# Optimization experiments

Hardware: AMD Instinct MI355X
Metric: run time of the kernel (lower is better)

The kernel has to match this reference:

```python
import jax, jax.numpy as jnp
import numpy as np

N = 100000   # nodes
E = 25000    # hyperedges
NNZ = 2000000
IN_CH = 64
HEADS = 8
OUT_CH = 8
HO = HEADS * OUT_CH  # 64


def setup_inputs() -> dict:
    key = jax.random.key(0)
    k1, k2, k3, k4, k5 = jax.random.split(key, 5)
    X = jax.random.normal(k1, (N, IN_CH), dtype=jnp.float32)
    vertex = jax.random.randint(k2, (NNZ,), 0, N, dtype=jnp.int64 if jax.config.jax_enable_x64 else jnp.int32)
    edges = jax.random.randint(k3, (NNZ,), 0, E, dtype=jnp.int64 if jax.config.jax_enable_x64 else jnp.int32)
    homo = jax.random.uniform(k4, (E,), dtype=jnp.float32) + 0.1  # positive per-hyperedge scalar
    # nn.Linear(in, heads*out, bias=False): store as [in, heads*out] for X @ W
    W = jax.random.normal(k5, (IN_CH, HO), dtype=jnp.float32) * (1.0 / np.sqrt(IN_CH))
    return {"X": X, "W": W, "homo": homo, "vertex": vertex, "edges": edges}


def reference(X, W, homo, vertex, edges):
    n = X.shape[0]
    e = homo.shape[0]
    Xp = X @ W                                   # [N, H*O]
    Xve = Xp[vertex]                             # [nnz, H*O] gather node->incidence
    # first_aggregate = 'mean': vertex features -> hyperedge features
    Xe_sum = jax.ops.segment_sum(Xve, edges, num_segments=e)
    cnt = jax.ops.segment_sum(jnp.ones((Xve.shape[0],), Xve.dtype), edges, num_segments=e)
    Xe = Xe_sum / jnp.maximum(cnt, 1.0)[:, None]  # [E, H*O]
    Xev = Xe[edges]                              # [nnz, H*O] gather edge->incidence
    he = homo[edges]                             # [nnz]
    att_sum = jax.ops.segment_sum(he, vertex, num_segments=n)[vertex]  # [nnz]
    att = he / att_sum                           # [nnz] (homo > 0 so sums > 0 at incident slots)
    att_Xev = att[:, None] * Xev                 # fused version of att.mm(ones).mul(Xev)
    # second_aggregate = 'sum': hyperedge features -> node features
    Xv = jax.ops.segment_sum(att_Xev, vertex, num_segments=n)  # [N, H*O]
    out = Xp + Xv
    # use_norm: row-l2 normalize with DETACHED norm (scale is a constant wrt grad)
    rownorm = jax.lax.stop_gradient(jnp.linalg.norm(out, axis=1, keepdims=True))
    scale = jnp.where(rownorm > 0, 1.0 / jnp.maximum(rownorm, 1e-30), 0.0)
    return out * scale
```

## Files before the change

### kernel.cpp

```cpp
#include <hip/hip_runtime.h>
#include <hip/hip_bf16.h>


#define SE_LOG 5
#define SV_LOG 7
#define CH     4096
#define CAPB   8192

typedef __attribute__((ext_vector_type(8))) short bf16x8;
typedef __attribute__((ext_vector_type(4))) float f32x4;

__device__ __forceinline__ float bf2f(unsigned short u) {
    union { unsigned int i; float f; } x;
    x.i = ((unsigned int)u) << 16;
    return x.f;
}

__device__ __forceinline__ float bflo(unsigned int u) {
    union { unsigned int i; float f; } x;
    x.i = u << 16;
    return x.f;
}

__device__ __forceinline__ float bfhi(unsigned int u) {
    union { unsigned int i; float f; } x;
    x.i = u & 0xffff0000u;
    return x.f;
}

__device__ __forceinline__ unsigned short f2bf(float f) {
    union { unsigned int i; float ff; } x;
    x.ff = f;
    unsigned int r = x.i + 0x7fff + ((x.i >> 16) & 1);
    return (unsigned short)(r >> 16);
}

__device__ __forceinline__ float loadF(const void* p, size_t i, int bf16mode) {
    return bf16mode ? bf2f(((const unsigned short*)p)[i]) : ((const float*)p)[i];
}

__device__ __forceinline__ int loadI(const void* p, size_t i, int i64mode) {
    return i64mode ? ((const int*)p)[2 * i] : ((const int*)p)[i];
}

__global__ void sniff_kernel(const void* X, const void* vtx, int* flags) {
    if (threadIdx.x != 0 || blockIdx.x != 0) return;
    const unsigned short* u = (const unsigned short*)X;
    int sane = 0;
    for (int i = 0; i < 64; ++i) {
        unsigned short lo = u[2 * i];
        int e = (lo >> 7) & 0xFF;
        if (e >= 110 && e <= 137) ++sane;
    }
    flags[0] = (sane >= 32) ? 1 : 0;
    const int* w = (const int*)vtx;
    int zeros = 0;
    for (int i = 0; i < 64; ++i)
        if (w[2 * i + 1] == 0) ++zeros;
    flags[1] = (zeros >= 32) ? 1 : 0;
}

__global__ void homof_kernel(const void* __restrict__ homo,
                             const int* __restrict__ flags,
                             float* __restrict__ homof, int E) {
    int i = blockIdx.x * blockDim.x + threadIdx.x;
    if (i < E) homof[i] = loadF(homo, i, flags[0]);
}

__global__ __launch_bounds__(256)
void gemm_mfma_kernel(const unsigned short* __restrict__ X,
                      const unsigned short* __restrict__ W,
                      const int* __restrict__ flags,
                      unsigned short* __restrict__ Xpb, int N) {
    if (flags[0] == 0) return;
    __shared__ float Ld[4][16 * 68];
    int tid  = threadIdx.x;
    int lane = tid & 63, w = tid >> 6;
    int quad = lane >> 4, c16 = lane & 15;
    bf16x8 bfrag[4][2];
#pragma unroll
    for (int t = 0; t < 4; ++t)
#pragma unroll
        for (int s = 0; s < 2; ++s)
#pragma unroll
            for (int j = 0; j < 8; ++j)
                bfrag[t][s][j] = (short)W[(s * 32 + quad * 8 + j) * 64 + t * 16 + c16];

    int tiles = (N + 15) >> 4;
    int wid = blockIdx.x * 4 + w;
    int nw  = gridDim.x * 4;
    int lr = lane >> 2, seg = lane & 3;
    for (int tile = wid; tile < tiles; tile += nw) {
        int r0 = tile * 16;
        int rA = r0 + c16; if (rA > N - 1) rA = N - 1;
        bf16x8 a0 = *(const bf16x8*)(X + (size_t)rA * 64 + quad * 8);
        bf16x8 a1 = *(const bf16x8*)(X + (size_t)rA * 64 + 32 + quad * 8);
#pragma unroll
        for (int t = 0; t < 4; ++t) {
            f32x4 z = {0.f, 0.f, 0.f, 0.f};
            z = __builtin_amdgcn_mfma_f32_16x16x32_bf16(a0, bfrag[t][0], z, 0, 0, 0);
            z = __builtin_amdgcn_mfma_f32_16x16x32_bf16(a1, bfrag[t][1], z, 0, 0, 0);
#pragma unroll
            for (int i = 0; i < 4; ++i)
                Ld[w][(quad * 4 + i) * 68 + t * 16 + c16] = z[i];
        }
        int r = r0 + lr;
        if (r < N) {
            const float* src = &Ld[w][lr * 68 + seg * 16];
            unsigned int p[8];
#pragma unroll
            for (int i = 0; i < 8; ++i)
                p[i] = (unsigned)f2bf(src[2 * i]) | ((unsigned)f2bf(src[2 * i + 1]) << 16);
            uint4* dst = (uint4*)(Xpb + (size_t)r * 64 + seg * 16);
            dst[0] = make_uint4(p[0], p[1], p[2], p[3]);
            dst[1] = make_uint4(p[4], p[5], p[6], p[7]);
        }
    }
}

__global__ __launch_bounds__(256)
void gemm_f32_kernel(const void* __restrict__ X, const void* __restrict__ W,
                     const int* __restrict__ flags,
                     unsigned short* __restrict__ Xpb, int N) {
    if (flags[0] == 1) return;
    __shared__ float Ws[64 * 64];
    __shared__ float Xs[16][64];
    int tid = threadIdx.x;
    for (int j = tid; j < 4096; j += 256) Ws[j] = ((const float*)W)[j];
    __syncthreads();
    int lane = tid & 63, w = tid >> 6;
    int wid = (blockIdx.x * 256 + tid) >> 6;
    int nw  = (gridDim.x * 256) >> 6;
    for (int r0 = wid * 4; r0 < N; r0 += nw * 4) {
        if (r0 + 4 <= N) {
            float acc0 = 0.f, acc1 = 0.f, acc2 = 0.f, acc3 = 0.f;
#pragma unroll
            for (int j = 0; j < 4; ++j)
                Xs[w * 4 + j][lane] = ((const float*)X)[(size_t)(r0 + j) * 64 + lane];
#pragma unroll
            for (int k4 = 0; k4 < 16; ++k4) {
                float4 x0 = *(const float4*)&Xs[w * 4 + 0][k4 * 4];
                float4 x1 = *(const float4*)&Xs[w * 4 + 1][k4 * 4];
                float4 x2 = *(const float4*)&Xs[w * 4 + 2][k4 * 4];
                float4 x3 = *(const float4*)&Xs[w * 4 + 3][k4 * 4];
#pragma unroll
                for (int kk = 0; kk < 4; ++kk) {
                    float wv = Ws[(k4 * 4 + kk) * 64 + lane];
                    acc0 = fmaf((&x0.x)[kk], wv, acc0);
                    acc1 = fmaf((&x1.x)[kk], wv, acc1);
                    acc2 = fmaf((&x2.x)[kk], wv, acc2);
                    acc3 = fmaf((&x3.x)[kk], wv, acc3);
                }
            }
            float a[4] = {acc0, acc1, acc2, acc3};
#pragma unroll
            for (int j = 0; j < 4; ++j)
                Xpb[(size_t)(r0 + j) * 64 + lane] = f2bf(a[j]);
        } else {
            for (int r = r0; r < N; ++r) {
                Xs[w * 4][lane] = ((const float*)X)[(size_t)r * 64 + lane];
                float acc = 0.f;
                for (int k = 0; k < 64; ++k)
                    acc = fmaf(Xs[w * 4][k], Ws[k * 64 + lane], acc);
                Xpb[(size_t)r * 64 + lane] = f2bf(acc);
            }
        }
    }
}

__global__ __launch_bounds__(1024)
void bhist2_kernel(const void* __restrict__ edges, const void* __restrict__ vertex,
                   const int* __restrict__ flags, int* __restrict__ btot,
                   int* __restrict__ slabc, int nnz, int NBE, int NBT) {
    __shared__ int cnt[2048];
    int tid = threadIdx.x, b = blockIdx.x;
    for (int j = tid; j < NBT; j += 1024) cnt[j] = 0;
    __syncthreads();
    int imode = flags[1];
    int c0 = b * CH, c1 = min(nnz, c0 + CH);
    for (int i = c0 + tid; i < c1; i += 1024) {
        int e = loadI(edges, i, imode);
        int v = loadI(vertex, i, imode);
        atomicAdd(&cnt[e >> SE_LOG], 1);
        atomicAdd(&cnt[NBE + (v >> SV_LOG)], 1);
    }
    __syncthreads();
    for (int j = tid; j < NBT; j += 1024) {
        int c = cnt[j];
        slabc[(size_t)b * NBT + j] = c;
        if (c) atomicAdd(&btot[j], c);
    }
}

__global__ void bscan_kernel(const int* __restrict__ btot, int* __restrict__ bbase,
                             int* __restrict__ bcur, int NBT) {
    __shared__ int wsum[16];
    __shared__ int carry_s;
    int tid = threadIdx.x, lane = tid & 63, w = tid >> 6;
    if (tid == 0) carry_s = 0;
    __syncthreads();
    for (int base = 0; base < NBT; base += 1024) {
        int i = base + tid;
        int x = (i < NBT) ? btot[i] : 0;
        int s = x;
#pragma unroll
        for (int d = 1; d < 64; d <<= 1) {
            int t = __shfl_up(s, d, 64);
            if (lane >= d) s += t;
        }
        if (lane == 63) wsum[w] = s;
        __syncthreads();
        if (w == 0 && lane < 16) {
            int v = wsum[lane];
#pragma unroll
            for (int d = 1; d < 16; d <<= 1) {
                int t = __shfl_up(v, d, 64);
                if (lane >= d) v += t;
            }
            wsum[lane] = v;
        }
        __syncthreads();
        int carry = carry_s;
        int excl  = carry + (w > 0 ? wsum[w - 1] : 0) + s - x;
        if (i < NBT) { bbase[i] = excl; bcur[i] = excl; }
        __syncthreads();
        if (tid == 1023) carry_s = carry + wsum[15];
        __syncthreads();
    }
    if (tid == 0) bbase[NBT] = carry_s;
}

__global__ __launch_bounds__(1024)
void bscatter2_kernel(const void* __restrict__ edges, const void* __restrict__ vertex,
                      const int* __restrict__ flags, int* __restrict__ bcur,
                      const int* __restrict__ slabc, int* __restrict__ buck,
                      int nnz, int NBE, int NBT, int bitsN, int bitsE) {
    __shared__ int cnt[2048];
    __shared__ int gb[2048];
    int tid = threadIdx.x, b = blockIdx.x;
    for (int j = tid; j < NBT; j += 1024) {
        int c = slabc[(size_t)b * NBT + j];
        gb[j]  = c ? atomicAdd(&bcur[j], c) : 0;
        cnt[j] = 0;
    }
    __syncthreads();
    int imode = flags[1];
    int c0 = b * CH, c1 = min(nnz, c0 + CH);
    for (int i = c0 + tid; i < c1; i += 1024) {
        int e = loadI(edges, i, imode);
        int v = loadI(vertex, i, imode);
        int be = e >> SE_LOG;
        int r  = atomicAdd(&cnt[be], 1);
        buck[gb[be] + r] = ((e & ((1 << SE_LOG) - 1)) << bitsN) | v;
        int bv = NBE + (v >> SV_LOG);
        int r2 = atomicAdd(&cnt[bv], 1);
        buck[gb[bv] + r2] = ((v & ((1 << SV_LOG) - 1)) << bitsE) | e;
    }
}

__global__ __launch_bounds__(512)
void bfe_kernel(const int* __restrict__ buck, const int* __restrict__ bbase,
                const float* __restrict__ homof, int* __restrict__ spill,
                const unsigned short* __restrict__ Xpb,
                unsigned short* __restrict__ Ye, int E, int bitsN) {
    __shared__ int list[CAPB];
    __shared__ int cnt[1 << SE_LOG];
    __shared__ int sexc[1 << SE_LOG];
    __shared__ int wsum[16];
    int g = blockIdx.x;
    int bin0 = g << SE_LOG;
    int nbins = min(1 << SE_LOG, E - bin0);
    int s0 = bbase[g], s1 = bbase[g + 1], size = s1 - s0;
    int tid = threadIdx.x, lane = tid & 63, w = tid >> 6;
    bool sp = (size > CAPB);
    int pmask = (1 << bitsN) - 1;
    if (tid < nbins) cnt[tid] = 0;
    __syncthreads();
    for (int j = tid; j < size; j += 512)
        atomicAdd(&cnt[buck[s0 + j] >> bitsN], 1);
    __syncthreads();
    {
        int x = (tid < nbins) ? cnt[tid] : 0;
        int s = x;
#pragma unroll
        for (int d = 1; d < 64; d <<= 1) {
            int t = __shfl_up(s, d, 64);
            if (lane >= d) s += t;
        }
        if (w == 0 && tid < nbins) sexc[tid] = s - x;
    }
    __syncthreads();
    if (tid < nbins) cnt[tid] = sexc[tid];
    __syncthreads();
    for (int j = tid; j < size; j += 512) {
        int p  = buck[s0 + j];
        int lb = p >> bitsN;
        int r  = atomicAdd(&cnt[lb], 1);
        int v  = p & pmask;
        if (sp) spill[s0 + r] = v; else list[r] = v;
    }
    __syncthreads();
    int grp = tid >> 4;
    int c = tid & 15;
    unsigned co = (unsigned)c << 3;
    if (grp < nbins) {
        int start = sexc[grp], end = cnt[grp];
        const char* Xb = (const char*)Xpb;
        float a0 = 0.f, a1 = 0.f, a2 = 0.f, a3 = 0.f;
        int j = start;
        if (!sp) {
            for (; j + 3 < end; j += 4) {
                int v0 = list[j], v1 = list[j + 1], v2 = list[j + 2], v3 = list[j + 3];
                uint2 u0 = *(const uint2*)(Xb + (((unsigned)v0 << 7) + co));
                uint2 u1 = *(const uint2*)(Xb + (((unsigned)v1 << 7) + co));
                uint2 u2 = *(const uint2*)(Xb + (((unsigned)v2 << 7) + co));
                uint2 u3 = *(const uint2*)(Xb + (((unsigned)v3 << 7) + co));
                a0 += (bflo(u0.x) + bflo(u1.x)) + (bflo(u2.x) + bflo(u3.x));
                a1 += (bfhi(u0.x) + bfhi(u1.x)) + (bfhi(u2.x) + bfhi(u3.x));
                a2 += (bflo(u0.y) + bflo(u1.y)) + (bflo(u2.y) + bflo(u3.y));
                a3 += (bfhi(u0.y) + bfhi(u1.y)) + (bfhi(u2.y) + bfhi(u3.y));
            }
            for (; j < end; ++j) {
                int v = list[j];
                uint2 u = *(const uint2*)(Xb + (((unsigned)v << 7) + co));
                a0 += bflo(u.x); a1 += bfhi(u.x);
                a2 += bflo(u.y); a3 += bfhi(u.y);
            }
        } else {
            for (; j < end; ++j) {
                int v = spill[s0 + j];
                uint2 u = *(const uint2*)(Xb + (((unsigned)v << 7) + co));
                a0 += bflo(u.x); a1 += bfhi(u.x);
                a2 += bflo(u.y); a3 += bfhi(u.y);
            }
        }
        int e = bin0 + grp;
        float inv = homof[e] / fmaxf((float)(end - start), 1.f);
        unsigned p0 = (unsigned)f2bf(a0 * inv) | ((unsigned)f2bf(a1 * inv) << 16);
        unsigned p1 = (unsigned)f2bf(a2 * inv) | ((unsigned)f2bf(a3 * inv) << 16);
        *(uint2*)((char*)Ye + (((unsigned)e << 7) + co)) = make_uint2(p0, p1);
    }
}

__global__ __launch_bounds__(512)
void bfv_kernel(const int* __restrict__ buck, const int* __restrict__ bbase,
                const float* __restrict__ homof, int* __restrict__ spill,
                const unsigned short* __restrict__ Xpb,
                const unsigned short* __restrict__ Ye,
                float* __restrict__ out, int N, int NBE, int bitsE) {
    __shared__ int list[CAPB];
    __shared__ int cnt[1 << SV_LOG];
    __shared__ int sexc[1 << SV_LOG];
    __shared__ float hsum[1 << SV_LOG];
    __shared__ int wsum[16];
    int bv = blockIdx.x;
    int bin0 = bv << SV_LOG;
    int nbins = min(1 << SV_LOG, N - bin0);
    int s0 = bbase[NBE + bv], s1 = bbase[NBE + bv + 1], size = s1 - s0;
    int tid = threadIdx.x, lane = tid & 63, w = tid >> 6;
    bool sp = (size > CAPB);
    int pmask = (1 << bitsE) - 1;
    if (tid < nbins) { cnt[tid] = 0; hsum[tid] = 0.f; }
    __syncthreads();
    for (int j = tid; j < size; j += 512)
        atomicAdd(&cnt[buck[s0 + j] >> bitsE], 1);
    __syncthreads();
    {
        int x = (tid < nbins) ? cnt[tid] : 0;
        int s = x;
#pragma unroll
        for (int d = 1; d < 64; d <<= 1) {
            int t = __shfl_up(s, d, 64);
            if (lane >= d) s += t;
        }
        if (lane == 63) wsum[w] = s;
        __syncthreads();
        if (w == 0 && lane < 16) {
            int v = wsum[lane];
#pragma unroll
            for (int d = 1; d < 16; d <<= 1) {
                int t = __shfl_up(v, d, 64);
                if (lane >= d) v += t;
            }
            wsum[lane] = v;
        }
        __syncthreads();
        int excl = s - x + (w > 0 ? wsum[w - 1] : 0);
        if (tid < nbins) sexc[tid] = excl;
    }
    __syncthreads();
    if (tid < nbins) cnt[tid] = sexc[tid];
    __syncthreads();
    for (int j = tid; j < size; j += 512) {
        int p  = buck[s0 + j];
        int lb = p >> bitsE;
        int r  = atomicAdd(&cnt[lb], 1);
        int e  = p & pmask;
        if (sp) spill[s0 + r] = e; else list[r] = e;
        atomicAdd(&hsum[lb], homof[e]);
    }
    __syncthreads();
    int grp = tid >> 3;
    int c = tid & 7;
    unsigned co = (unsigned)c << 4;
    const char* Yb = (const char*)Ye;
    for (int vl = grp; vl < nbins; vl += 64) {
        int start = sexc[vl], end = cnt[vl];
        float a0 = 0.f, a1 = 0.f, a2 = 0.f, a3 = 0.f;
        float a4 = 0.f, a5 = 0.f, a6 = 0.f, a7 = 0.f;
        int j = start;
        if (!sp) {
            for (; j + 3 < end; j += 4) {
                int e0 = list[j], e1 = list[j + 1], e2 = list[j + 2], e3 = list[j + 3];
                uint4 u0 = *(const uint4*)(Yb + (((unsigned)e0 << 7) + co));
                uint4 u1 = *(const uint4*)(Yb + (((unsigned)e1 << 7) + co));
                uint4 u2 = *(const uint4*)(Yb + (((unsigned)e2 << 7) + co));
                uint4 u3 = *(const uint4*)(Yb + (((unsigned)e3 << 7) + co));
                a0 += (bflo(u0.x) + bflo(u1.x)) + (bflo(u2.x) + bflo(u3.x));
                a1 += (bfhi(u0.x) + bfhi(u1.x)) + (bfhi(u2.x) + bfhi(u3.x));
                a2 += (bflo(u0.y) + bflo(u1.y)) + (bflo(u2.y) + bflo(u3.y));
                a3 += (bfhi(u0.y) + bfhi(u1.y)) + (bfhi(u2.y) + bfhi(u3.y));
                a4 += (bflo(u0.z) + bflo(u1.z)) + (bflo(u2.z) + bflo(u3.z));
                a5 += (bfhi(u0.z) + bfhi(u1.z)) + (bfhi(u2.z) + bfhi(u3.z));
                a6 += (bflo(u0.w) + bflo(u1.w)) + (bflo(u2.w) + bflo(u3.w));
                a7 += (bfhi(u0.w) + bfhi(u1.w)) + (bfhi(u2.w) + bfhi(u3.w));
            }
            for (; j < end; ++j) {
                int e = list[j];
                uint4 u = *(const uint4*)(Yb + (((unsigned)e << 7) + co));
                a0 += bflo(u.x); a1 += bfhi(u.x);
                a2 += bflo(u.y); a3 += bfhi(u.y);
                a4 += bflo(u.z); a5 += bfhi(u.z);
                a6 += bflo(u.w); a7 += bfhi(u.w);
            }
        } else {
            for (; j < end; ++j) {
                int e = spill[s0 + j];
                uint4 u = *(const uint4*)(Yb + (((unsigned)e << 7) + co));
                a0 += bflo(u.x); a1 += bfhi(u.x);
                a2 += bflo(u.y); a3 += bfhi(u.y);
                a4 += bflo(u.z); a5 += bfhi(u.z);
                a6 += bflo(u.w); a7 += bfhi(u.w);
            }
        }
        int vid = bin0 + vl;
        float hsv = hsum[vl];
        float inv = (hsv > 0.f) ? 1.f / hsv : 0.f;
        uint4 xu = *(const uint4*)((const char*)Xpb + (((unsigned)vid << 7) + co));
        float r0 = bflo(xu.x) + a0 * inv, r1 = bfhi(xu.x) + a1 * inv;
        float r2 = bflo(xu.y) + a2 * inv, r3 = bfhi(xu.y) + a3 * inv;
        float r4 = bflo(xu.z) + a4 * inv, r5 = bfhi(xu.z) + a5 * inv;
        float r6 = bflo(xu.w) + a6 * inv, r7 = bfhi(xu.w) + a7 * inv;
        float ss = ((r0 * r0 + r1 * r1) + (r2 * r2 + r3 * r3)) +
                   ((r4 * r4 + r5 * r5) + (r6 * r6 + r7 * r7));
        ss += __shfl_xor(ss, 1, 64);
        ss += __shfl_xor(ss, 2, 64);
        ss += __shfl_xor(ss, 4, 64);
        float rn    = sqrtf(ss);
        float scale = (rn > 0.f) ? 1.f / fmaxf(rn, 1e-30f) : 0.f;
        char* ob = (char*)out + (((unsigned)vid << 8) + (co << 1));
        *(float4*)ob        = make_float4(r0 * scale, r1 * scale, r2 * scale, r3 * scale);
        *(float4*)(ob + 16) = make_float4(r4 * scale, r5 * scale, r6 * scale, r7 * scale);
    }
}

__global__ void hist_atomic_kernel(const void* __restrict__ edges,
                                   const void* __restrict__ vertex,
                                   const int* __restrict__ flags,
                                   int* __restrict__ tot, int E, int nnz) {
    int i = blockIdx.x * blockDim.x + threadIdx.x;
    if (i >= nnz) return;
    int imode = flags[1];
    atomicAdd(&tot[loadI(edges, i, imode)], 1);
    atomicAdd(&tot[E + loadI(vertex, i, imode)], 1);
}

__global__ void scan_part_kernel(const int* __restrict__ tot, int* __restrict__ part, int M) {
    int g = blockIdx.x, tid = threadIdx.x;
    int base = g * 2048;
    int sum = 0;
    for (int j = tid; j < 2048; j += 256) {
        int i = base + j;
        sum += (i < M) ? tot[i] : 0;
    }
#pragma unroll
    for (int d = 32; d >= 1; d >>= 1) sum += __shfl_xor(sum, d, 64);
    __shared__ int wsums[4];
    int lane = tid & 63, w = tid >> 6;
    if (lane == 0) wsums[w] = sum;
    __syncthreads();
    if (tid == 0) part[g] = wsums[0] + wsums[1] + wsums[2] + wsums[3];
}

__global__ void scan_root_kernel(int* __restrict__ part, int G,
                                 int* __restrict__ off, int M) {
    int tid = threadIdx.x, lane = tid & 63, w = tid >> 6;
    int x = (tid < G) ? part[tid] : 0;
    int s = x;
#pragma unroll
    for (int d = 1; d < 64; d <<= 1) {
        int t = __shfl_up(s, d, 64);
        if (lane >= d) s += t;
    }
    __shared__ int ws[16];
    if (lane == 63) ws[w] = s;
    __syncthreads();
    if (w == 0 && lane < 16) {
        int v = ws[lane];
#pragma unroll
        for (int d = 1; d < 16; d <<= 1) {
            int t = __shfl_up(v, d, 64);
            if (lane >= d) v += t;
        }
        ws[lane] = v;
    }
    __syncthreads();
    int excl = s - x + (w > 0 ? ws[w - 1] : 0);
    if (tid < G) part[tid] = excl;
    if (tid == 1023) off[M] = ws[15];
}

__global__ void scan_apply_kernel(int* __restrict__ tot, const int* __restrict__ part,
                                  int* __restrict__ off, int M) {
    int g = blockIdx.x, tid = threadIdx.x, lane = tid & 63, w = tid >> 6;
    int base = g * 2048 + tid * 8;
    int e[8]; int s = 0;
#pragma unroll
    for (int j = 0; j < 8; ++j) {
        int i = base + j;
        e[j] = (i < M) ? tot[i] : 0;
        s += e[j];
    }
    int si = s;
#pragma unroll
    for (int d = 1; d < 64; d <<= 1) {
        int t = __shfl_up(si, d, 64);
        if (lane >= d) si += t;
    }
    __shared__ int wsum[4];
    if (lane == 63) wsum[w] = si;
    __syncthreads();
    int wbase = 0;
    for (int ww = 0; ww < w; ++ww) wbase += wsum[ww];
    int run = part[g] + wbase + si - s;
#pragma unroll
    for (int j = 0; j < 8; ++j) {
        int i = base + j;
        if (i < M) off[i] = run;
        run += e[j];
    }
}

__global__ void copy_kernel(const int* __restrict__ src, int* __restrict__ dst, int n) {
    int i = blockIdx.x * blockDim.x + threadIdx.x;
    if (i < n) dst[i] = src[i];
}

__global__ void scatter_atomic_kernel(const void* __restrict__ edges,
                                      const void* __restrict__ vertex,
                                      const int* __restrict__ flags,
                                      int* __restrict__ cur, int* __restrict__ dest,
                                      int E, int nnz) {
    int i = blockIdx.x * blockDim.x + threadIdx.x;
    if (i >= nnz) return;
    int imode = flags[1];
    int e = loadI(edges, i, imode);
    int v = loadI(vertex, i, imode);
    dest[atomicAdd(&cur[e], 1)]     = v;
    dest[atomicAdd(&cur[E + v], 1)] = e;
}

__global__ void hs_fallback_kernel(const int* __restrict__ off,
                                   const int* __restrict__ sorted,
                                   const float* __restrict__ homof,
                                   float* __restrict__ hs, int E, int N) {
    int v = blockIdx.x * blockDim.x + threadIdx.x;
    if (v >= N) return;
    int s = off[E + v], e = off[E + v + 1];
    float t = 0.f;
    for (int j = s; j < e; ++j) t += homof[sorted[j]];
    hs[v] = t;
}

__global__ void edge_mean_kernel(const unsigned short* __restrict__ Xpb,
                                 const int* __restrict__ off,
                                 const int* __restrict__ sorted,
                                 const float* __restrict__ homof,
                                 unsigned short* __restrict__ Ye, int E) {
    int wid  = (blockIdx.x * blockDim.x + threadIdx.x) >> 6;
    int lane = threadIdx.x & 63;
    if (wid >= E) return;
    int g = lane >> 4, c = lane & 15;
    unsigned co = (unsigned)c << 3;
    int start = off[wid], end = off[wid + 1];
    float a0 = 0.f, a1 = 0.f, a2 = 0.f, a3 = 0.f;
    const char* Xb = (const char*)Xpb;
    for (int j = start + g; j < end; j += 4) {
        int v = sorted[j];
        uint2 u = *(const uint2*)(Xb + (((unsigned)v << 7) + co));
        a0 += bflo(u.x); a1 += bfhi(u.x);
        a2 += bflo(u.y); a3 += bfhi(u.y);
    }
    a0 += __shfl_xor(a0, 16, 64); a0 += __shfl_xor(a0, 32, 64);
    a1 += __shfl_xor(a1, 16, 64); a1 += __shfl_xor(a1, 32, 64);
    a2 += __shfl_xor(a2, 16, 64); a2 += __shfl_xor(a2, 32, 64);
    a3 += __shfl_xor(a3, 16, 64); a3 += __shfl_xor(a3, 32, 64);
    if (g == 0) {
        float inv = homof[wid] / fmaxf((float)(end - start), 1.f);
        unsigned p0 = (unsigned)f2bf(a0 * inv) | ((unsigned)f2bf(a1 * inv) << 16);
        unsigned p1 = (unsigned)f2bf(a2 * inv) | ((unsigned)f2bf(a3 * inv) << 16);
        *(uint2*)((char*)Ye + (((unsigned)wid << 7) + co)) = make_uint2(p0, p1);
    }
}

__global__ void vertex_out_kernel(const unsigned short* __restrict__ Xpb,
                                  const unsigned short* __restrict__ Ye,
                                  const int* __restrict__ off,
                                  const int* __restrict__ sorted,
                                  const float* __restrict__ hs,
                                  float* __restrict__ out, int E, int N) {
    int wv   = (blockIdx.x * blockDim.x + threadIdx.x) >> 6;
    int lane = threadIdx.x & 63;
    int g = lane >> 3, c = lane & 7;
    int vid = wv * 8 + g;
    if (vid >= N) return;
    unsigned co = (unsigned)c << 4;
    int start = off[E + vid], end = off[E + vid + 1];
    float a0 = 0.f, a1 = 0.f, a2 = 0.f, a3 = 0.f;
    float a4 = 0.f, a5 = 0.f, a6 = 0.f, a7 = 0.f;
    const char* Yb = (const char*)Ye;
    for (int j = start; j < end; ++j) {
        int e = sorted[j];
        uint4 u = *(const uint4*)(Yb + (((unsigned)e << 7) + co));
        a0 += bflo(u.x); a1 += bfhi(u.x);
        a2 += bflo(u.y); a3 += bfhi(u.y);
        a4 += bflo(u.z); a5 += bfhi(u.z);
        a6 += bflo(u.w); a7 += bfhi(u.w);
    }
    float hsv = hs[vid];
    float inv = (hsv > 0.f) ? 1.f / hsv : 0.f;
    uint4 xu = *(const uint4*)((const char*)Xpb + (((unsigned)vid << 7) + co));
    float r0 = bflo(xu.x) + a0 * inv, r1 = bfhi(xu.x) + a1 * inv;
    float r2 = bflo(xu.y) + a2 * inv, r3 = bfhi(xu.y) + a3 * inv;
    float r4 = bflo(xu.z) + a4 * inv, r5 = bfhi(xu.z) + a5 * inv;
    float r6 = bflo(xu.w) + a6 * inv, r7 = bfhi(xu.w) + a7 * inv;
    float ss = ((r0 * r0 + r1 * r1) + (r2 * r2 + r3 * r3)) +
               ((r4 * r4 + r5 * r5) + (r6 * r6 + r7 * r7));
    ss += __shfl_xor(ss, 1, 64);
    ss += __shfl_xor(ss, 2, 64);
    ss += __shfl_xor(ss, 4, 64);
    float rn    = sqrtf(ss);
    float scale = (rn > 0.f) ? 1.f / fmaxf(rn, 1e-30f) : 0.f;
    char* ob = (char*)out + (((unsigned)vid << 8) + (co << 1));
    *(float4*)ob        = make_float4(r0 * scale, r1 * scale, r2 * scale, r3 * scale);
    *(float4*)(ob + 16) = make_float4(r4 * scale, r5 * scale, r6 * scale, r7 * scale);
}

static inline int ceil_bits(int n) {
    int v = n - 1;
    if (v < 1) v = 1;
    int b = 0;
    while ((1 << b) <= v) ++b;
    return b;
}

extern "C" void kernel_launch(void* const* d_in, const int* in_sizes, int n_in,
                              void* d_out, int out_size, void* d_ws, size_t ws_size,
                              hipStream_t stream) {
    const void* X      = d_in[0];
    const void* W      = d_in[1];
    const void* homo   = d_in[2];
    const void* vertex = d_in[3];
    const void* edges  = d_in[4];
    float* out = (float*)d_out;

    const int N   = in_sizes[0] / 64;
    const int E   = in_sizes[2];
    const int NNZ = in_sizes[3];
    const int M   = E + N;

    const int NBE = (E + (1 << SE_LOG) - 1) >> SE_LOG;
    const int NBV = (N + (1 << SV_LOG) - 1) >> SV_LOG;
    const int NBT = NBE + NBV;
    const int GC  = (NNZ + CH - 1) / CH;
    const int bitsN = ceil_bits(N);
    const int bitsE = ceil_bits(E);
    const int G   = (M + 2047) / 2048;

    char*  ws = (char*)d_ws;
    size_t o  = 0;
    auto alloc = [&](size_t bytes) -> void* {
        void* p = ws + o;
        o += (bytes + 255) & ~(size_t)255;
        return p;
    };
    int*            flags = (int*)alloc(2 * 4);
    int*            bbase = (int*)alloc((size_t)(NBT + 1) * 4);
    int*            bcur  = (int*)alloc((size_t)NBT * 4);
    int*            btot  = (int*)alloc((size_t)NBT * 4);
    float*          homof = (float*)alloc((size_t)E * 4);
    int*            buck  = (int*)alloc((size_t)2 * NNZ * 4);
    int*            spill = (int*)alloc((size_t)2 * NNZ * 4);
    unsigned short* Xpb   = (unsigned short*)alloc((size_t)N * 64 * 2);
    unsigned short* Ye    = (unsigned short*)alloc((size_t)E * 64 * 2);
    int*            slabc = (int*)alloc((size_t)GC * NBT * 4);
    size_t o_common = o;
    bool fast = (o <= ws_size) && NBT <= 2048 &&
                (SE_LOG + bitsN <= 31) && (SV_LOG + bitsE <= 31) && G <= 1024;
    (void)n_in; (void)out_size;

    sniff_kernel<<<1, 64, 0, stream>>>(X, vertex, flags);
    homof_kernel<<<(E + 255) / 256, 256, 0, stream>>>(homo, flags, homof, E);
    gemm_mfma_kernel<<<1024, 256, 0, stream>>>((const unsigned short*)X,
                                               (const unsigned short*)W,
                                               flags, Xpb, N);
    gemm_f32_kernel<<<512, 256, 0, stream>>>(X, W, flags, Xpb, N);

    if (fast) {
        hipMemsetAsync(btot, 0, (size_t)NBT * 4, stream);
        bhist2_kernel<<<GC, 1024, 0, stream>>>(edges, vertex, flags, btot,
                                               slabc, NNZ, NBE, NBT);
        bscan_kernel<<<1, 1024, 0, stream>>>(btot, bbase, bcur, NBT);
        bscatter2_kernel<<<GC, 1024, 0, stream>>>(edges, vertex, flags, bcur,
                                                  slabc, buck, NNZ, NBE, NBT,
                                                  bitsN, bitsE);
        bfe_kernel<<<NBE, 512, 0, stream>>>(buck, bbase, homof, spill,
                                            Xpb, Ye, E, bitsN);
        bfv_kernel<<<NBV, 512, 0, stream>>>(buck, bbase, homof, spill,
                                            Xpb, Ye, out, N, NBE, bitsE);
    } else {
        o = o_common;
        int* off  = (int*)alloc((size_t)(M + 1) * 4);
        float* hs = (float*)alloc((size_t)N * 4);
        int* tot  = (int*)alloc((size_t)M * 4);
        int* part = (int*)alloc((size_t)(G + 1) * 4);
        int* cur  = (int*)alloc((size_t)M * 4);
        int* sorted = spill;
        hipMemsetAsync(tot, 0, (size_t)M * 4, stream);
        int nb = (NNZ + 255) / 256;
        hist_atomic_kernel<<<nb, 256, 0, stream>>>(edges, vertex, flags, tot, E, NNZ);
        scan_part_kernel<<<G, 256, 0, stream>>>(tot, part, M);
        scan_root_kernel<<<1, 1024, 0, stream>>>(part, G, off, M);
        scan_apply_kernel<<<G, 256, 0, stream>>>(tot, part, off, M);
        copy_kernel<<<(M + 255) / 256, 256, 0, stream>>>(off, cur, M);
        scatter_atomic_kernel<<<nb, 256, 0, stream>>>(edges, vertex, flags, cur, sorted, E, NNZ);
        hs_fallback_kernel<<<(N + 255) / 256, 256, 0, stream>>>(off, sorted, homof, hs, E, N);
        edge_mean_kernel<<<(E + 3) / 4, 256, 0, stream>>>(Xpb, off, sorted, homof, Ye, E);
        int vwaves  = (N + 7) / 8;
        int vblocks = (vwaves * 64 + 255) / 256;
        vertex_out_kernel<<<vblocks, 256, 0, stream>>>(Xpb, Ye, off, sorted, hs, out, E, N);
    }
}
```

Measured before the change: 262.1 us.

## Double bucket width and split each bucket across two half-blocks

Coarsens the edge and vertex bucketing (SE_LOG 5→6, SV_LOG 7→8) so the scatter phase handles fewer, larger buckets. Each bucket is then processed by two blocks, each filtering the entries for its half of the bins. The aim is to cut per-bucket overhead in histogram, scan and scatter while keeping per-block bin counts and shared-memory lists the same size. In exchange, every entry of a bucket is read twice (once per half), and larger buckets are more likely to overflow CAPB and take the slower spill path. A no-op null check on X was also added to the gemm_f32 weight load.

```diff
diff --git a/kernel.cpp b/kernel.cpp
--- a/kernel.cpp
+++ b/kernel.cpp
@@ -2,8 +2,8 @@
 #include <hip/hip_bf16.h>
 
 
-#define SE_LOG 5
-#define SV_LOG 7
+#define SE_LOG 6
+#define SV_LOG 8
 #define CH     4096
 #define CAPB   8192
 
@@ -126,7 +126,7 @@
     __shared__ float Ws[64 * 64];
     __shared__ float Xs[16][64];
     int tid = threadIdx.x;
-    for (int j = tid; j < 4096; j += 256) Ws[j] = ((const float*)W)[j];
+    for (int j = tid; j < 4096; j += 256) Ws[j] = ((const float*)X == nullptr) ? 0.f : ((const float*)W)[j];
     __syncthreads();
     int lane = tid & 63, w = tid >> 6;
     int wid = (blockIdx.x * 256 + tid) >> 6;
@@ -264,46 +264,57 @@
                 const unsigned short* __restrict__ Xpb,
                 unsigned short* __restrict__ Ye, int E, int bitsN) {
     __shared__ int list[CAPB];
-    __shared__ int cnt[1 << SE_LOG];
-    __shared__ int sexc[1 << SE_LOG];
-    __shared__ int wsum[16];
-    int g = blockIdx.x;
-    int bin0 = g << SE_LOG;
-    int nbins = min(1 << SE_LOG, E - bin0);
+    __shared__ int cnt[32];
+    __shared__ int sexc[32];
+    __shared__ int tot_s;
+    int blk = blockIdx.x;
+    int g = blk >> 1, half = blk & 1;
+    int bin0f = g << SE_LOG;
+    int nbf   = min(1 << SE_LOG, E - bin0f);
+    int hb0   = half * 32;
+    int nbh   = nbf - hb0; if (nbh > 32) nbh = 32;
+    if (nbh <= 0) return;
     int s0 = bbase[g], s1 = bbase[g + 1], size = s1 - s0;
     int tid = threadIdx.x, lane = tid & 63, w = tid >> 6;
-    bool sp = (size > CAPB);
     int pmask = (1 << bitsN) - 1;
-    if (tid < nbins) cnt[tid] = 0;
-    __syncthreads();
-    for (int j = tid; j < size; j += 512)
-        atomicAdd(&cnt[buck[s0 + j] >> bitsN], 1);
-    __syncthreads();
-    {
-        int x = (tid < nbins) ? cnt[tid] : 0;
+    if (tid < nbh) cnt[tid] = 0;
+    __syncthreads();
+    for (int j = tid; j < size; j += 512) {
+        int lb = (buck[s0 + j] >> bitsN) - hb0;
+        if ((unsigned)lb < (unsigned)nbh) atomicAdd(&cnt[lb], 1);
+    }
+    __syncthreads();
+    if (w == 0) {
+        int x = (lane < nbh) ? cnt[lane] : 0;
         int s = x;
 #pragma unroll
         for (int d = 1; d < 64; d <<= 1) {
             int t = __shfl_up(s, d, 64);
             if (lane >= d) s += t;
         }
-        if (w == 0 && tid < nbins) sexc[tid] = s - x;
-    }
-    __syncthreads();
-    if (tid < nbins) cnt[tid] = sexc[tid];
+        if (lane < nbh) sexc[lane] = s - x;
+        if (lane == nbh - 1) tot_s = s;
+    }
+    __syncthreads();
+    int halfsize = tot_s;
+    bool sp = (halfsize > CAPB);
+    int soff = s0 + (half ? (size - halfsize) : 0);
+    if (tid < nbh) cnt[tid] = sexc[tid];
     __syncthreads();
     for (int j = tid; j < size; j += 512) {
         int p  = buck[s0 + j];
-        int lb = p >> bitsN;
-        int r  = atomicAdd(&cnt[lb], 1);
-        int v  = p & pmask;
-        if (sp) spill[s0 + r] = v; else list[r] = v;
+        int lb = (p >> bitsN) - hb0;
+        if ((unsigned)lb < (unsigned)nbh) {
+            int r = atomicAdd(&cnt[lb], 1);
+            int v = p & pmask;
+            if (sp) spill[soff + r] = v; else list[r] = v;
+        }
     }
     __syncthreads();
     int grp = tid >> 4;
     int c = tid & 15;
     unsigned co = (unsigned)c << 3;
-    if (grp < nbins) {
+    if (grp < nbh) {
         int start = sexc[grp], end = cnt[grp];
         const char* Xb = (const char*)Xpb;
         float a0 = 0.f, a1 = 0.f, a2 = 0.f, a3 = 0.f;
@@ -328,13 +339,13 @@
             }
         } else {
             for (; j < end; ++j) {
-                int v = spill[s0 + j];
+                int v = spill[soff + j];
                 uint2 u = *(const uint2*)(Xb + (((unsigned)v << 7) + co));
                 a0 += bflo(u.x); a1 += bfhi(u.x);
                 a2 += bflo(u.y); a3 += bfhi(u.y);
             }
         }
-        int e = bin0 + grp;
+        int e = bin0f + hb0 + grp;
         float inv = homof[e] / fmaxf((float)(end - start), 1.f);
         unsigned p0 = (unsigned)f2bf(a0 * inv) | ((unsigned)f2bf(a1 * inv) << 16);
         unsigned p1 = (unsigned)f2bf(a2 * inv) | ((unsigned)f2bf(a3 * inv) << 16);
@@ -349,24 +360,30 @@
                 const unsigned short* __restrict__ Ye,
                 float* __restrict__ out, int N, int NBE, int bitsE) {
     __shared__ int list[CAPB];
-    __shared__ int cnt[1 << SV_LOG];
-    __shared__ int sexc[1 << SV_LOG];
-    __shared__ float hsum[1 << SV_LOG];
-    __shared__ int wsum[16];
-    int bv = blockIdx.x;
-    int bin0 = bv << SV_LOG;
-    int nbins = min(1 << SV_LOG, N - bin0);
+    __shared__ int cnt[128];
+    __shared__ int sexc[128];
+    __shared__ float hsum[128];
+    __shared__ int wsum[8];
+    __shared__ int tot_s;
+    int blk = blockIdx.x;
+    int bv = blk >> 1, half = blk & 1;
+    int bin0f = bv << SV_LOG;
+    int nbf   = min(1 << SV_LOG, N - bin0f);
+    int hb0   = half * 128;
+    int nbh   = nbf - hb0; if (nbh > 128) nbh = 128;
+    if (nbh <= 0) return;
     int s0 = bbase[NBE + bv], s1 = bbase[NBE + bv + 1], size = s1 - s0;
     int tid = threadIdx.x, lane = tid & 63, w = tid >> 6;
-    bool sp = (size > CAPB);
     int pmask = (1 << bitsE) - 1;
-    if (tid < nbins) { cnt[tid] = 0; hsum[tid] = 0.f; }
-    __syncthreads();
-    for (int j = tid; j < size; j += 512)
-        atomicAdd(&cnt[buck[s0 + j] >> bitsE], 1);
+    if (tid < nbh) { cnt[tid] = 0; hsum[tid] = 0.f; }
+    __syncthreads();
+    for (int j = tid; j < size; j += 512) {
+        int lb = (buck[s0 + j] >> bitsE) - hb0;
+        if ((unsigned)lb < (unsigned)nbh) atomicAdd(&cnt[lb], 1);
+    }
     __syncthreads();
     {
-        int x = (tid < nbins) ? cnt[tid] : 0;
+        int x = (tid < nbh) ? cnt[tid] : 0;
         int s = x;
 #pragma unroll
         for (int d = 1; d < 64; d <<= 1) {
@@ -375,10 +392,10 @@
         }
         if (lane == 63) wsum[w] = s;
         __syncthreads();
-        if (w == 0 && lane < 16) {
+        if (w == 0 && lane < 8) {
             int v = wsum[lane];
 #pragma unroll
-            for (int d = 1; d < 16; d <<= 1) {
+            for (int d = 1; d < 8; d <<= 1) {
                 int t = __shfl_up(v, d, 64);
                 if (lane >= d) v += t;
             }
@@ -386,25 +403,31 @@
         }
         __syncthreads();
         int excl = s - x + (w > 0 ? wsum[w - 1] : 0);
-        if (tid < nbins) sexc[tid] = excl;
-    }
-    __syncthreads();
-    if (tid < nbins) cnt[tid] = sexc[tid];
+        if (tid < nbh) sexc[tid] = excl;
+        if (tid == nbh - 1) tot_s = excl + x;
+    }
+    __syncthreads();
+    int halfsize = tot_s;
+    bool sp = (halfsize > CAPB);
+    int soff = s0 + (half ? (size - halfsize) : 0);
+    if (tid < nbh) cnt[tid] = sexc[tid];
     __syncthreads();
     for (int j = tid; j < size; j += 512) {
         int p  = buck[s0 + j];
-        int lb = p >> bitsE;
-        int r  = atomicAdd(&cnt[lb], 1);
-        int e  = p & pmask;
-        if (sp) spill[s0 + r] = e; else list[r] = e;
-        atomicAdd(&hsum[lb], homof[e]);
+        int lb = (p >> bitsE) - hb0;
+        if ((unsigned)lb < (unsigned)nbh) {
+            int r = atomicAdd(&cnt[lb], 1);
+            int e = p & pmask;
+            if (sp) spill[soff + r] = e; else list[r] = e;
+            atomicAdd(&hsum[lb], homof[e]);
+        }
     }
     __syncthreads();
     int grp = tid >> 3;
     int c = tid & 7;
     unsigned co = (unsigned)c << 4;
     const char* Yb = (const char*)Ye;
-    for (int vl = grp; vl < nbins; vl += 64) {
+    for (int vl = grp; vl < nbh; vl += 64) {
         int start = sexc[vl], end = cnt[vl];
         float a0 = 0.f, a1 = 0.f, a2 = 0.f, a3 = 0.f;
         float a4 = 0.f, a5 = 0.f, a6 = 0.f, a7 = 0.f;
@@ -435,7 +458,7 @@
             }
         } else {
             for (; j < end; ++j) {
-                int e = spill[s0 + j];
+                int e = spill[soff + j];
                 uint4 u = *(const uint4*)(Yb + (((unsigned)e << 7) + co));
                 a0 += bflo(u.x); a1 += bfhi(u.x);
                 a2 += bflo(u.y); a3 += bfhi(u.y);
@@ -443,7 +466,7 @@
                 a6 += bflo(u.w); a7 += bfhi(u.w);
             }
         }
-        int vid = bin0 + vl;
+        int vid = bin0f + hb0 + vl;
         float hsv = hsum[vl];
         float inv = (hsv > 0.f) ? 1.f / hsv : 0.f;
         uint4 xu = *(const uint4*)((const char*)Xpb + (((unsigned)vid << 7) + co));
@@ -724,10 +747,10 @@
         bscatter2_kernel<<<GC, 1024, 0, stream>>>(edges, vertex, flags, bcur,
                                                   slabc, buck, NNZ, NBE, NBT,
                                                   bitsN, bitsE);
-        bfe_kernel<<<NBE, 512, 0, stream>>>(buck, bbase, homof, spill,
-                                            Xpb, Ye, E, bitsN);
-        bfv_kernel<<<NBV, 512, 0, stream>>>(buck, bbase, homof, spill,
-                                            Xpb, Ye, out, N, NBE, bitsE);
+        bfe_kernel<<<2 * NBE, 512, 0, stream>>>(buck, bbase, homof, spill,
+                                                Xpb, Ye, E, bitsN);
+        bfv_kernel<<<2 * NBV, 512, 0, stream>>>(buck, bbase, homof, spill,
+                                                Xpb, Ye, out, N, NBE, bitsE);
     } else {
         o = o_common;
         int* off  = (int*)alloc((size_t)(M + 1) * 4);
```

Result: no change. 259.4 us (-1.0%).
